# Performance work log

Hardware: AMD Instinct MI355X
Metric: run time of the kernel (lower is better)

## Reference

```python
import jax, jax.numpy as jnp
import numpy as np

B, L, F, H, U = 512, 64, 2048, 512, 512


def setup_inputs() -> dict:
    key = jax.random.key(0)
    ks = jax.random.split(key, 10)
    s = 0.05
    return {
        'features': jax.random.normal(ks[0], (B, L, F), jnp.float32),
        'hidden': jax.random.normal(ks[1], (B, H), jnp.float32),
        'W1': jax.random.normal(ks[2], (F, U), jnp.float32) * s,
        'b1': jnp.zeros((U,), jnp.float32),
        'W2': jax.random.normal(ks[3], (H, U), jnp.float32) * s,
        'b2': jnp.zeros((U,), jnp.float32),
        'V': jax.random.normal(ks[4], (U, 1), jnp.float32) * s,
        'bV': jnp.zeros((1,), jnp.float32),
        'W3': jax.random.normal(ks[5], (F + H, U), jnp.float32) * s,
        'b3': jnp.zeros((U,), jnp.float32),
        'ka1': jax.random.normal(ks[6], (H, L), jnp.float32) * s,
        'kb1': jax.random.normal(ks[7], (L, L), jnp.float32) * s,
        'ka2': jax.random.normal(ks[8], (H, L), jnp.float32) * s,
        'kb2': jax.random.normal(ks[9], (L, L), jnp.float32) * s,
    }


def reference(features, hidden, W1, b1, W2, b2, V, bV, W3, b3, ka1, kb1, ka2, kb2):
    # features: [B, L, F], hidden: [B, H]
    Lp = features.shape[1]
    h = hidden[:, None, :]  # [B, 1, H] = hidden_with_time_axis

    # score_model == 'default'
    score = jnp.tanh(features @ W1 + b1 + (h @ W2 + b2))  # [B, L, U]
    logits = score @ V + bV  # [B, L, 1]
    attention_weights = jax.nn.softmax(logits, axis=1)  # [B, L, 1]

    # local_att == 'True': Gaussian window re-weighting (vectorized version of
    # the original nested Python loops over (batch, position)).
    def local_p(ka, kb):
        t = jnp.tanh(h @ ka) @ kb  # [B, 1, L]
        t = jax.nn.sigmoid(t) * jnp.sqrt(jnp.float32(Lp))
        return jnp.transpose(t, (0, 2, 1))  # [B, L, 1]

    p1 = local_p(ka1, kb1)  # predicted row center, [B, L, 1]
    p2 = local_p(ka2, kb2)  # predicted col center, [B, L, 1]

    i = jnp.arange(Lp, dtype=jnp.float32)
    g = jnp.sqrt(jnp.float32(Lp))
    rows = jnp.floor((i + 1.0) / g)                 # s_t[..., 0]
    cols = jnp.floor(jnp.mod(i + 1.0, g)) - 1.0     # s_t[..., 1]
    d2 = (rows[None, :, None] - p1) ** 2 + (cols[None, :, None] - p2) ** 2  # [B, L, 1]

    D = 1.0
    attention_weights = attention_weights * jnp.exp(-d2 / (0.5 * D * D))

    context_vector = jnp.sum(attention_weights * features, axis=1)  # [B, F]

    # context_vector_concat == 'True'
    out = jnp.tanh(jnp.concatenate([context_vector, hidden], axis=-1)) @ W3 + b3  # [B, U]
    return out, attention_weights
```

## Files before the change

### kernel.cpp

```cpp
#include <hip/hip_runtime.h>

typedef __bf16 bf16x8 __attribute__((ext_vector_type(8)));
typedef float f32x4 __attribute__((ext_vector_type(4)));

static __device__ __forceinline__ unsigned short f2bf(float f) {
  union { float fv; unsigned u; } v; v.fv = f;
  unsigned u = v.u;
  u += 0x7fffu + ((u >> 16) & 1u);
  return (unsigned short)(u >> 16);
}

static __device__ __forceinline__ int4 pack8(const float4& x0, const float4& x1) {
  union { unsigned short u[8]; int4 v; } r;
  r.u[0] = f2bf(x0.x); r.u[1] = f2bf(x0.y); r.u[2] = f2bf(x0.z); r.u[3] = f2bf(x0.w);
  r.u[4] = f2bf(x1.x); r.u[5] = f2bf(x1.y); r.u[6] = f2bf(x1.z); r.u[7] = f2bf(x1.w);
  return r.v;
}

static __device__ __forceinline__ float fast_tanh(float x) {
  x = fminf(fmaxf(x, -15.f), 15.f);
  float ex = __expf(2.f * x);
  return (ex - 1.f) / (ex + 1.f);
}

__global__ __launch_bounds__(256) void pack_all(
    const float* __restrict__ W1, const float* __restrict__ W2,
    const float* __restrict__ W3,
    unsigned short* __restrict__ W1p, unsigned short* __restrict__ W2p,
    unsigned short* __restrict__ W3p) {
  __shared__ float tile[32][65];
  const int N = 512;
  const float* W; unsigned short* P; int nk;
  if (blockIdx.z == 0)      { W = W1; P = W1p; nk = 64; }
  else if (blockIdx.z == 1) { W = W2; P = W2p; nk = 16; }
  else                      { W = W3; P = W3p; nk = 80; }
  if ((int)blockIdx.x >= nk) return;
  int k0 = blockIdx.x * 32, n0 = blockIdx.y * 64;
  int t = threadIdx.x;
  int nn = t & 63, kkb = t >> 6;
#pragma unroll
  for (int i = 0; i < 8; ++i) {
    int kk = kkb + i * 4;
    tile[kk][nn] = W[(size_t)(k0 + kk) * N + n0 + nn];
  }
  __syncthreads();
#pragma unroll
  for (int i = 0; i < 8; ++i) {
    int e = t + i * 256;
    int k8 = e & 7, n = (e >> 3) & 63, c = e >> 9;
    size_t dst = (size_t)((k0 >> 3) + c) * 4096 + (size_t)(n0 + n) * 8 + k8;
    P[dst] = f2bf(tile[c * 8 + k8][n]);
  }
}

__global__ __launch_bounds__(128) void prep_batch(
    const float* __restrict__ hidden,
    const float* __restrict__ ka1, const float* __restrict__ kb1,
    const float* __restrict__ ka2, const float* __restrict__ kb2,
    float* __restrict__ gauss,
    unsigned short* __restrict__ hid_bf,
    unsigned short* __restrict__ A2) {
  int b = blockIdx.x, t = threadIdx.x;
  __shared__ float hl[512];
  __shared__ float tt[128];
  __shared__ float pp[128];
  for (int i = t; i < 512; i += 128) {
    float v = hidden[b * 512 + i];
    hl[i] = v;
    hid_bf[b * 512 + i] = f2bf(v);
    A2[(size_t)b * 2560 + 2048 + i] = f2bf(tanhf(v));
  }
  __syncthreads();
  {
    const float* ka = (t < 64) ? ka1 : ka2;
    int lp = t & 63;
    float s0 = 0.f, s1 = 0.f, s2 = 0.f, s3 = 0.f;
    for (int h = 0; h < 512; h += 4) {
      s0 += hl[h + 0] * ka[(h + 0) * 64 + lp];
      s1 += hl[h + 1] * ka[(h + 1) * 64 + lp];
      s2 += hl[h + 2] * ka[(h + 2) * 64 + lp];
      s3 += hl[h + 3] * ka[(h + 3) * 64 + lp];
    }
    tt[t] = tanhf((s0 + s1) + (s2 + s3));
  }
  __syncthreads();
  {
    const float* kb = (t < 64) ? kb1 : kb2;
    const float* ts = (t < 64) ? tt : tt + 64;
    int l = t & 63;
    float s = 0.f;
    for (int j = 0; j < 64; ++j) s += ts[j] * kb[j * 64 + l];
    pp[t] = 8.0f / (1.0f + expf(-s));
  }
  __syncthreads();
  if (t < 64) {
    float fi = (float)(t + 1);
    float r = floorf(fi * 0.125f);
    float c = floorf(fmodf(fi, 8.0f)) - 1.0f;
    float dr = r - pp[t], dc = c - pp[64 + t];
    gauss[b * 64 + t] = expf(-2.0f * (dr * dr + dc * dc));
  }
}

__global__ __launch_bounds__(256, 2) void gemm64d(
    const unsigned short* __restrict__ A, int lda, int k8_stride, int nsteps,
    const unsigned short* __restrict__ Wp,
    const float* __restrict__ bias,
    float* __restrict__ C) {
  __shared__ unsigned short lA[2][64 * 40];
  int m0 = blockIdx.x * 64, n0 = blockIdx.y * 64;
  int z = blockIdx.z;
  int k8 = z * k8_stride;
  int t = threadIdx.x;
  int w = t >> 6, lane = t & 63, q = lane >> 4, l15 = lane & 15;
  f32x4 acc[4] = {};
  int arow = t >> 2, achk = (t & 3) * 8;
  const unsigned short* pA = A + (size_t)(m0 + arow) * lda + (size_t)k8 * 8 + achk;
  const unsigned short* pB = Wp + ((size_t)(k8 + q) * 512 + n0 + w * 16 + l15) * 8;
  *(int4*)(&lA[0][arow * 40 + achk]) = *(const int4*)(pA);
  __syncthreads();
  for (int ks = 0; ks < nsteps; ++ks) {
    int p = ks & 1;
    int4 bv = *(const int4*)(pB + (size_t)ks * 16384);
    int ksn = (ks < nsteps - 1) ? ks + 1 : ks;
    int4 av = *(const int4*)(pA + ksn * 32);
    bf16x8 af[4];
#pragma unroll
    for (int mt = 0; mt < 4; ++mt)
      af[mt] = *(const bf16x8*)(&lA[p][(mt * 16 + l15) * 40 + q * 8]);
    bf16x8 bf = *(const bf16x8*)&bv;
#pragma unroll
    for (int mt = 0; mt < 4; ++mt)
      acc[mt] = __builtin_amdgcn_mfma_f32_16x16x32_bf16(af[mt], bf, acc[mt], 0, 0, 0);
    *(int4*)(&lA[1 - p][arow * 40 + achk]) = av;
    __syncthreads();
  }
  int col = n0 + w * 16 + l15;
  if (bias) {
    float bsv = bias[col];
#pragma unroll
    for (int mt = 0; mt < 4; ++mt)
#pragma unroll
      for (int j = 0; j < 4; ++j)
        C[(size_t)(m0 + mt * 16 + q * 4 + j) * 512 + col] = acc[mt][j] + bsv;
  } else {
    float* Cp = C + (size_t)z * 262144;
#pragma unroll
    for (int mt = 0; mt < 4; ++mt)
#pragma unroll
      for (int j = 0; j < 4; ++j)
        Cp[(size_t)(m0 + mt * 16 + q * 4 + j) * 512 + col] = acc[mt][j];
  }
}

__global__ __launch_bounds__(256) void reduce4(const float* __restrict__ part,
                                               const float* __restrict__ b3,
                                               float* __restrict__ out) {
  int i = blockIdx.x * 256 + threadIdx.x;
  int base = i * 4;
  int n = base & 511;
  float4 p0 = *(const float4*)(part + base);
  float4 p1 = *(const float4*)(part + 262144 + base);
  float4 p2 = *(const float4*)(part + 524288 + base);
  float4 p3 = *(const float4*)(part + 786432 + base);
  float4 bv = *(const float4*)(b3 + n);
  float4 r;
  r.x = p0.x + p1.x + p2.x + p3.x + bv.x;
  r.y = p0.y + p1.y + p2.y + p3.y + bv.y;
  r.z = p0.z + p1.z + p2.z + p3.z + bv.z;
  r.w = p0.w + p1.w + p2.w + p3.w + bv.w;
  *(float4*)(out + base) = r;
}

__global__ __launch_bounds__(256, 2) void attn_main(
    const float* __restrict__ feat,
    const unsigned short* __restrict__ W1p,
    const float* __restrict__ b1,
    const float* __restrict__ hb,
    const float* __restrict__ V,
    const float* __restrict__ bVp,
    const float* __restrict__ gauss,
    float* __restrict__ aw_out,
    unsigned short* __restrict__ A2) {
  __shared__ unsigned short lA[2][64 * 72];
  __shared__ float red[64 * 4];
  __shared__ float awl[64];
  int b = blockIdx.x, t = threadIdx.x;
  int w = t >> 6, lane = t & 63, q = lane >> 4, l15 = lane & 15;
  f32x4 acc[4][8] = {};
  int arow = t >> 2, aseg = (t & 3) * 16;
  const float* Ab = feat + (size_t)b * (64 * 2048);
  const float* pA = Ab + (size_t)arow * 2048 + aseg;
  const unsigned short* pB = W1p + ((size_t)q * 512 + w * 128 + l15) * 8;
  int wA = arow * 72 + aseg;

  float vv[8], bb[8];
#pragma unroll
  for (int nt = 0; nt < 8; ++nt) {
    int u = w * 128 + nt * 16 + l15;
    vv[nt] = V[u];
    bb[nt] = b1[u] + hb[b * 512 + u];
  }
  float gs = (t < 64) ? gauss[b * 64 + t] : 0.f;
  float bV0 = bVp[0];

  {
    float4 x0 = *(const float4*)(pA + 0);
    float4 x1 = *(const float4*)(pA + 4);
    float4 x2 = *(const float4*)(pA + 8);
    float4 x3 = *(const float4*)(pA + 12);
    *(int4*)(&lA[0][wA])     = pack8(x0, x1);
    *(int4*)(&lA[0][wA + 8]) = pack8(x2, x3);
  }
  __syncthreads();

  for (int s = 0; s < 32; ++s) {
    int p = s & 1;
    const unsigned short* bp = pB + (size_t)s * 32768;
    int4 bfr[16];
#pragma unroll
    for (int i = 0; i < 16; ++i)
      bfr[i] = *(const int4*)(bp + (i >> 3) * 16384 + (i & 7) * 128);
    int sn = (s < 31) ? s + 1 : 31;
    const float* pn = pA + sn * 64;
    float4 x0 = *(const float4*)(pn + 0);
    float4 x1 = *(const float4*)(pn + 4);
    float4 x2 = *(const float4*)(pn + 8);
    float4 x3 = *(const float4*)(pn + 12);
    bf16x8 af[4][2];
#pragma unroll
    for (int mt = 0; mt < 4; ++mt)
#pragma unroll
      for (int kh = 0; kh < 2; ++kh)
        af[mt][kh] = *(const bf16x8*)(&lA[p][(mt * 16 + l15) * 72 + kh * 32 + q * 8]);
#pragma unroll
    for (int kh = 0; kh < 2; ++kh)
#pragma unroll
      for (int mt = 0; mt < 4; ++mt)
#pragma unroll
        for (int nt = 0; nt < 8; ++nt)
          acc[mt][nt] = __builtin_amdgcn_mfma_f32_16x16x32_bf16(
              af[mt][kh], *(const bf16x8*)&bfr[kh * 8 + nt], acc[mt][nt], 0, 0, 0);
    *(int4*)(&lA[1 - p][wA])     = pack8(x0, x1);
    *(int4*)(&lA[1 - p][wA + 8]) = pack8(x2, x3);
    __syncthreads();
  }

#pragma unroll
  for (int mt = 0; mt < 4; ++mt) {
#pragma unroll
    for (int j = 0; j < 4; ++j) {
      float pv = 0.f;
#pragma unroll
      for (int nt = 0; nt < 8; ++nt)
        pv += fast_tanh(acc[mt][nt][j] + bb[nt]) * vv[nt];
      pv += __shfl_xor(pv, 1);
      pv += __shfl_xor(pv, 2);
      pv += __shfl_xor(pv, 4);
      pv += __shfl_xor(pv, 8);
      if (l15 == 0) red[(mt * 16 + q * 4 + j) * 4 + w] = pv;
    }
  }
  __syncthreads();
  if (t < 64) {
    float s = bV0 + red[t * 4] + red[t * 4 + 1] + red[t * 4 + 2] + red[t * 4 + 3];
    float mx = s;
#pragma unroll
    for (int o = 1; o < 64; o <<= 1) mx = fmaxf(mx, __shfl_xor(mx, o));
    float e = __expf(s - mx);
    float sm = e;
#pragma unroll
    for (int o = 1; o < 64; o <<= 1) sm += __shfl_xor(sm, o);
    float a = (e / sm) * gs;
    awl[t] = a;
    aw_out[b * 64 + t] = a;
  }
  __syncthreads();
  float4 c0 = make_float4(0.f, 0.f, 0.f, 0.f);
  float4 c1 = make_float4(0.f, 0.f, 0.f, 0.f);
  const float* pF = Ab + t * 8;
#pragma unroll 4
  for (int l = 0; l < 64; ++l) {
    float a = awl[l];
    float4 f0 = *(const float4*)(pF + l * 2048);
    float4 f1 = *(const float4*)(pF + l * 2048 + 4);
    c0.x += a * f0.x; c0.y += a * f0.y; c0.z += a * f0.z; c0.w += a * f0.w;
    c1.x += a * f1.x; c1.y += a * f1.y; c1.z += a * f1.z; c1.w += a * f1.w;
  }
  ushort4 o0, o1;
  o0.x = f2bf(fast_tanh(c0.x)); o0.y = f2bf(fast_tanh(c0.y));
  o0.z = f2bf(fast_tanh(c0.z)); o0.w = f2bf(fast_tanh(c0.w));
  o1.x = f2bf(fast_tanh(c1.x)); o1.y = f2bf(fast_tanh(c1.y));
  o1.z = f2bf(fast_tanh(c1.z)); o1.w = f2bf(fast_tanh(c1.w));
  *(ushort4*)(A2 + (size_t)b * 2560 + t * 8) = o0;
  *(ushort4*)(A2 + (size_t)b * 2560 + t * 8 + 4) = o1;
}

extern "C" void kernel_launch(void* const* d_in, const int* in_sizes, int n_in,
                              void* d_out, int out_size, void* d_ws, size_t ws_size,
                              hipStream_t stream) {
  (void)in_sizes; (void)n_in; (void)out_size; (void)ws_size;
  const float* feat   = (const float*)d_in[0];
  const float* hidden = (const float*)d_in[1];
  const float* W1  = (const float*)d_in[2];
  const float* b1  = (const float*)d_in[3];
  const float* W2  = (const float*)d_in[4];
  const float* b2  = (const float*)d_in[5];
  const float* V   = (const float*)d_in[6];
  const float* bV  = (const float*)d_in[7];
  const float* W3  = (const float*)d_in[8];
  const float* b3  = (const float*)d_in[9];
  const float* ka1 = (const float*)d_in[10];
  const float* kb1 = (const float*)d_in[11];
  const float* ka2 = (const float*)d_in[12];
  const float* kb2 = (const float*)d_in[13];

  char* ws = (char*)d_ws;
  unsigned short* W3p   = (unsigned short*)(ws);
  unsigned short* A2    = (unsigned short*)(ws + 2621440);
  unsigned short* W1p   = (unsigned short*)(ws + 5242880);
  unsigned short* W2p   = (unsigned short*)(ws + 7340032);
  unsigned short* hidbf = (unsigned short*)(ws + 7864320);
  float*          hb    = (float*)(ws + 8388608);
  float*          gauss = (float*)(ws + 9437184);
  float*          part  = (float*)(ws + 5242880);

  float* out    = (float*)d_out;
  float* aw_out = out + 512 * 512;

  pack_all<<<dim3(80, 8, 3), 256, 0, stream>>>(W1, W2, W3, W1p, W2p, W3p);
  prep_batch<<<512, 128, 0, stream>>>(hidden, ka1, kb1, ka2, kb2, gauss, hidbf, A2);
  gemm64d<<<dim3(8, 8, 1), 256, 0, stream>>>(hidbf, 512, 0, 16, W2p, b2, hb);
  attn_main<<<512, 256, 0, stream>>>(feat, W1p, b1, hb, V, bV, gauss, aw_out, A2);
  gemm64d<<<dim3(8, 8, 4), 256, 0, stream>>>(A2, 2560, 80, 20, W3p, nullptr, part);
  reduce4<<<256, 256, 0, stream>>>(part, b3, out);
}
```

Measured before the change: 525.3 us.

## Drop LDS staging in attn_main; use 512 threads with 2x4 wave tiling

The attention GEMM block grows from 4 to 8 waves, arranged 2 (M) by 4 (N). Each wave now loads its own A fragments straight from global fp32 features into registers and converts them to bf16 there, replacing the double-buffered LDS tile and the per-step __syncthreads. This removes LDS traffic and barriers and raises occupancy. In exchange, two waves that share N columns each load the same W1 rows, so W1 traffic doubles, and the A loads are strided fragment reads with no prefetch beyond unroll 2. The weighted context sum is re-split so each of the 512 threads covers 4 features.

New measurement: 615.3 us. 1.17x slower.

```diff
diff --git a/kernel.cpp b/kernel.cpp
--- a/kernel.cpp
+++ b/kernel.cpp
@@ -10,8 +10,8 @@
   return (unsigned short)(u >> 16);
 }
 
-static __device__ __forceinline__ int4 pack8(const float4& x0, const float4& x1) {
-  union { unsigned short u[8]; int4 v; } r;
+static __device__ __forceinline__ bf16x8 pack8bf(const float4& x0, const float4& x1) {
+  union { unsigned short u[8]; bf16x8 v; } r;
   r.u[0] = f2bf(x0.x); r.u[1] = f2bf(x0.y); r.u[2] = f2bf(x0.z); r.u[3] = f2bf(x0.w);
   r.u[4] = f2bf(x1.x); r.u[5] = f2bf(x1.y); r.u[6] = f2bf(x1.z); r.u[7] = f2bf(x1.w);
   return r.v;
@@ -172,7 +172,7 @@
   *(float4*)(out + base) = r;
 }
 
-__global__ __launch_bounds__(256, 2) void attn_main(
+__global__ __launch_bounds__(512, 4) void attn_main(
     const float* __restrict__ feat,
     const unsigned short* __restrict__ W1p,
     const float* __restrict__ b1,
@@ -182,72 +182,57 @@
     const float* __restrict__ gauss,
     float* __restrict__ aw_out,
     unsigned short* __restrict__ A2) {
-  __shared__ unsigned short lA[2][64 * 72];
   __shared__ float red[64 * 4];
   __shared__ float awl[64];
   int b = blockIdx.x, t = threadIdx.x;
   int w = t >> 6, lane = t & 63, q = lane >> 4, l15 = lane & 15;
-  f32x4 acc[4][8] = {};
-  int arow = t >> 2, aseg = (t & 3) * 16;
+  int wm = w >> 2, wn = w & 3;
+  f32x4 acc[2][8] = {};
   const float* Ab = feat + (size_t)b * (64 * 2048);
-  const float* pA = Ab + (size_t)arow * 2048 + aseg;
-  const unsigned short* pB = W1p + ((size_t)q * 512 + w * 128 + l15) * 8;
-  int wA = arow * 72 + aseg;
+  const float* pA0 = Ab + (size_t)(wm * 32 + l15) * 2048 + q * 8;
+  const float* pA1 = pA0 + 16 * 2048;
+  const unsigned short* pB = W1p + ((size_t)q * 512 + wn * 128 + l15) * 8;
+
+#pragma unroll 2
+  for (int k0 = 0; k0 < 2048; k0 += 32) {
+    float4 a00 = *(const float4*)(pA0 + k0);
+    float4 a01 = *(const float4*)(pA0 + k0 + 4);
+    float4 a10 = *(const float4*)(pA1 + k0);
+    float4 a11 = *(const float4*)(pA1 + k0 + 4);
+    const unsigned short* bp = pB + (size_t)k0 * 512;
+    int4 bh[4];
+#pragma unroll
+    for (int nt = 0; nt < 4; ++nt) bh[nt] = *(const int4*)(bp + nt * 128);
+    bf16x8 a0 = pack8bf(a00, a01);
+    bf16x8 a1 = pack8bf(a10, a11);
+#pragma unroll
+    for (int nt = 0; nt < 4; ++nt) {
+      bf16x8 bf = *(const bf16x8*)&bh[nt];
+      acc[0][nt] = __builtin_amdgcn_mfma_f32_16x16x32_bf16(a0, bf, acc[0][nt], 0, 0, 0);
+      acc[1][nt] = __builtin_amdgcn_mfma_f32_16x16x32_bf16(a1, bf, acc[1][nt], 0, 0, 0);
+    }
+#pragma unroll
+    for (int nt = 0; nt < 4; ++nt) bh[nt] = *(const int4*)(bp + (nt + 4) * 128);
+#pragma unroll
+    for (int nt = 0; nt < 4; ++nt) {
+      bf16x8 bf = *(const bf16x8*)&bh[nt];
+      acc[0][nt + 4] = __builtin_amdgcn_mfma_f32_16x16x32_bf16(a0, bf, acc[0][nt + 4], 0, 0, 0);
+      acc[1][nt + 4] = __builtin_amdgcn_mfma_f32_16x16x32_bf16(a1, bf, acc[1][nt + 4], 0, 0, 0);
+    }
+  }
 
   float vv[8], bb[8];
 #pragma unroll
   for (int nt = 0; nt < 8; ++nt) {
-    int u = w * 128 + nt * 16 + l15;
+    int u = wn * 128 + nt * 16 + l15;
     vv[nt] = V[u];
     bb[nt] = b1[u] + hb[b * 512 + u];
   }
   float gs = (t < 64) ? gauss[b * 64 + t] : 0.f;
   float bV0 = bVp[0];
 
-  {
-    float4 x0 = *(const float4*)(pA + 0);
-    float4 x1 = *(const float4*)(pA + 4);
-    float4 x2 = *(const float4*)(pA + 8);
-    float4 x3 = *(const float4*)(pA + 12);
-    *(int4*)(&lA[0][wA])     = pack8(x0, x1);
-    *(int4*)(&lA[0][wA + 8]) = pack8(x2, x3);
-  }
-  __syncthreads();
-
-  for (int s = 0; s < 32; ++s) {
-    int p = s & 1;
-    const unsigned short* bp = pB + (size_t)s * 32768;
-    int4 bfr[16];
-#pragma unroll
-    for (int i = 0; i < 16; ++i)
-      bfr[i] = *(const int4*)(bp + (i >> 3) * 16384 + (i & 7) * 128);
-    int sn = (s < 31) ? s + 1 : 31;
-    const float* pn = pA + sn * 64;
-    float4 x0 = *(const float4*)(pn + 0);
-    float4 x1 = *(const float4*)(pn + 4);
-    float4 x2 = *(const float4*)(pn + 8);
-    float4 x3 = *(const float4*)(pn + 12);
-    bf16x8 af[4][2];
-#pragma unroll
-    for (int mt = 0; mt < 4; ++mt)
-#pragma unroll
-      for (int kh = 0; kh < 2; ++kh)
-        af[mt][kh] = *(const bf16x8*)(&lA[p][(mt * 16 + l15) * 72 + kh * 32 + q * 8]);
-#pragma unroll
-    for (int kh = 0; kh < 2; ++kh)
-#pragma unroll
-      for (int mt = 0; mt < 4; ++mt)
-#pragma unroll
-        for (int nt = 0; nt < 8; ++nt)
-          acc[mt][nt] = __builtin_amdgcn_mfma_f32_16x16x32_bf16(
-              af[mt][kh], *(const bf16x8*)&bfr[kh * 8 + nt], acc[mt][nt], 0, 0, 0);
-    *(int4*)(&lA[1 - p][wA])     = pack8(x0, x1);
-    *(int4*)(&lA[1 - p][wA + 8]) = pack8(x2, x3);
-    __syncthreads();
-  }
-
-#pragma unroll
-  for (int mt = 0; mt < 4; ++mt) {
+#pragma unroll
+  for (int mt = 0; mt < 2; ++mt) {
 #pragma unroll
     for (int j = 0; j < 4; ++j) {
       float pv = 0.f;
@@ -258,7 +243,7 @@
       pv += __shfl_xor(pv, 2);
       pv += __shfl_xor(pv, 4);
       pv += __shfl_xor(pv, 8);
-      if (l15 == 0) red[(mt * 16 + q * 4 + j) * 4 + w] = pv;
+      if (l15 == 0) red[(wm * 32 + mt * 16 + q * 4 + j) * 4 + wn] = pv;
     }
   }
   __syncthreads();
@@ -277,23 +262,17 @@
   }
   __syncthreads();
   float4 c0 = make_float4(0.f, 0.f, 0.f, 0.f);
-  float4 c1 = make_float4(0.f, 0.f, 0.f, 0.f);
-  const float* pF = Ab + t * 8;
+  const float* pF = Ab + t * 4;
 #pragma unroll 4
   for (int l = 0; l < 64; ++l) {
     float a = awl[l];
     float4 f0 = *(const float4*)(pF + l * 2048);
-    float4 f1 = *(const float4*)(pF + l * 2048 + 4);
     c0.x += a * f0.x; c0.y += a * f0.y; c0.z += a * f0.z; c0.w += a * f0.w;
-    c1.x += a * f1.x; c1.y += a * f1.y; c1.z += a * f1.z; c1.w += a * f1.w;
-  }
-  ushort4 o0, o1;
+  }
+  ushort4 o0;
   o0.x = f2bf(fast_tanh(c0.x)); o0.y = f2bf(fast_tanh(c0.y));
   o0.z = f2bf(fast_tanh(c0.z)); o0.w = f2bf(fast_tanh(c0.w));
-  o1.x = f2bf(fast_tanh(c1.x)); o1.y = f2bf(fast_tanh(c1.y));
-  o1.z = f2bf(fast_tanh(c1.z)); o1.w = f2bf(fast_tanh(c1.w));
-  *(ushort4*)(A2 + (size_t)b * 2560 + t * 8) = o0;
-  *(ushort4*)(A2 + (size_t)b * 2560 + t * 8 + 4) = o1;
+  *(ushort4*)(A2 + (size_t)b * 2560 + t * 4) = o0;
 }
 
 extern "C" void kernel_launch(void* const* d_in, const int* in_sizes, int n_in,
@@ -331,7 +310,7 @@
   pack_all<<<dim3(80, 8, 3), 256, 0, stream>>>(W1, W2, W3, W1p, W2p, W3p);
   prep_batch<<<512, 128, 0, stream>>>(hidden, ka1, kb1, ka2, kb2, gauss, hidbf, A2);
   gemm64d<<<dim3(8, 8, 1), 256, 0, stream>>>(hidbf, 512, 0, 16, W2p, b2, hb);
-  attn_main<<<512, 256, 0, stream>>>(feat, W1p, b1, hb, V, bV, gauss, aw_out, A2);
+  attn_main<<<512, 512, 0, stream>>>(feat, W1p, b1, hb, V, bV, gauss, aw_out, A2);
   gemm64d<<<dim3(8, 8, 4), 256, 0, stream>>>(A2, 2560, 80, 20, W3p, nullptr, part);
   reduce4<<<256, 256, 0, stream>>>(part, b3, out);
 }
```
